# Kernel optimization log

Hardware: AMD Instinct MI355X
Metric: run time of the kernel (lower is better)

## Reference

```python
import jax, jax.numpy as jnp
import numpy as np

B, C, H, W = 16, 192, 48, 48
EPS = 1e-5  # torch LayerNorm default


def setup_inputs() -> dict:
    key = jax.random.key(0)
    ks = jax.random.split(key, 5)
    dim = C
    x = jax.random.normal(ks[0], (B, C, H, W), dtype=jnp.float32)
    ln_w = jnp.ones((dim,), dtype=jnp.float32)
    ln_b = jnp.zeros((dim,), dtype=jnp.float32)
    s = 1.0 / np.sqrt(dim)
    Wq = jax.random.uniform(ks[1], (dim, dim), jnp.float32, -s, s)
    Wk = jax.random.uniform(ks[2], (dim, dim), jnp.float32, -s, s)
    Wv = jax.random.uniform(ks[3], (dim, dim), jnp.float32, -s, s)
    w1 = jnp.ones((1,), dtype=jnp.float32)
    w2 = jnp.ones((1,), dtype=jnp.float32)
    return {"x": x, "ln_w": ln_w, "ln_b": ln_b, "Wq": Wq, "Wk": Wk, "Wv": Wv, "w1": w1, "w2": w2}


def reference(x, ln_w, ln_b, Wq, Wk, Wv, w1, w2):
    b, c, h, w = x.shape
    # [B, C, H, W] -> [B, N, C]
    xf = x.reshape(b, c, h * w).transpose(0, 2, 1)
    # LayerNorm over channel dim
    mu = jnp.mean(xf, axis=-1, keepdims=True)
    var = jnp.mean(jnp.square(xf - mu), axis=-1, keepdims=True)
    xn = (xf - mu) * jax.lax.rsqrt(var + EPS) * ln_w + ln_b
    # torch Linear: y = x @ W^T
    Q = jnp.einsum('bnc,dc->bnd', xn, Wq)
    K = jnp.einsum('bnc,dc->bnd', xn, Wk)
    V = jnp.einsum('bnc,dc->bnd', xn, Wv)
    S = jnp.einsum('bnd,bmd->bnm', Q, K)  # [B, N, N]
    attn1 = jax.nn.softmax(S, axis=-1)
    attn2 = jnp.square(jax.nn.relu(S))
    # learned blend weights (softmax over two scalars)
    e1, e2 = jnp.exp(w1), jnp.exp(w2)
    denom = e1 + e2
    attn = (e1 / denom) * attn1 + (e2 / denom) * attn2
    out = jnp.einsum('bnm,bmd->bnd', attn, V)  # [B, N, C]
    out = out.transpose(0, 2, 1).reshape(b, c, h, w)
    return out + x
```

## Files before the change

kernel.cpp:

```cpp
#include <hip/hip_runtime.h>

#define NN 2304
#define CC 192
#define NBATCH 16

typedef unsigned short u16;
typedef __bf16 bf16x8 __attribute__((ext_vector_type(8)));
typedef float f32x4 __attribute__((ext_vector_type(4)));
typedef float f32x16 __attribute__((ext_vector_type(16)));

__device__ __forceinline__ u16 bf16bits(float f) {
  union { float f; unsigned u; } v;
  v.f = f;
  unsigned r = v.u + 0x7FFFu + ((v.u >> 16) & 1u);
  return (u16)(r >> 16);
}

__device__ __forceinline__ int swzK(int row, int col) {
  int ch = col >> 3;
  int phys = (ch & ~7) | ((ch ^ row) & 7);
  return row * 192 + (phys << 3) + (col & 7);
}
__device__ __forceinline__ int swz64(int row, int col) {
  int ch = (col >> 3) ^ row;
  return (row << 6) | ((ch & 7) << 3) | (col & 7);
}

__device__ __forceinline__ void gll16(const u16* g, u16* l) {
  __builtin_amdgcn_global_load_lds(
      (const __attribute__((address_space(1))) u16*)g,
      (__attribute__((address_space(3))) u16*)l, 16, 0, 0);
}

__global__ __launch_bounds__(256) void ln_kernel(
    const float* __restrict__ x, const float* __restrict__ lnw,
    const float* __restrict__ lnb, u16* __restrict__ xn) {
  __shared__ float xt[192 * 65];
  __shared__ float psum[4][64], psq[4][64];
  __shared__ float mu_s[64], rs_s[64];
  __shared__ float lw_s[192], lb_s[192];
  int t = threadIdx.x;
  int b = blockIdx.y, n0 = blockIdx.x * 64;
  const float* xb = x + (size_t)b * CC * NN;
  if (t < 192) { lw_s[t] = lnw[t]; lb_s[t] = lnb[t]; }
#pragma unroll
  for (int i = 0; i < 48; ++i) {
    int idx = i * 256 + t;
    int c = idx >> 6, n = idx & 63;
    xt[c * 65 + n] = xb[(size_t)c * NN + n0 + n];
  }
  __syncthreads();
  {
    int n = t & 63, part = t >> 6;
    float s = 0.f, s2 = 0.f;
#pragma unroll
    for (int c = part * 48; c < part * 48 + 48; ++c) {
      float v = xt[c * 65 + n];
      s += v; s2 += v * v;
    }
    psum[part][n] = s; psq[part][n] = s2;
  }
  __syncthreads();
  if (t < 64) {
    float s = psum[0][t] + psum[1][t] + psum[2][t] + psum[3][t];
    float s2 = psq[0][t] + psq[1][t] + psq[2][t] + psq[3][t];
    float mu = s * (1.0f / 192.0f);
    float var = s2 * (1.0f / 192.0f) - mu * mu;
    mu_s[t] = mu;
    rs_s[t] = rsqrtf(var + 1e-5f);
  }
  __syncthreads();
#pragma unroll
  for (int i = 0; i < 12; ++i) {
    int u = i * 256 + t;
    int n = u / 48, cq = (u % 48) * 4;
    float mu = mu_s[n], rs = rs_s[n];
    alignas(8) u16 tmp[4];
#pragma unroll
    for (int k2 = 0; k2 < 4; ++k2) {
      float v = (xt[(cq + k2) * 65 + n] - mu) * rs * lw_s[cq + k2] + lb_s[cq + k2];
      tmp[k2] = bf16bits(v);
    }
    *(uint2*)&xn[((size_t)(b * NN + n0 + n)) * CC + cq] = *(uint2*)tmp;
  }
}

__global__ __launch_bounds__(256, 3) void qkv_gemm(
    const u16* __restrict__ xn, const float* __restrict__ Wq,
    const float* __restrict__ Wk, const float* __restrict__ Wv,
    u16* __restrict__ qb, u16* __restrict__ kb, u16* __restrict__ vtb) {
  __shared__ u16 xs[12288];
  __shared__ u16 wsm[12288];
  int t = threadIdx.x, w = t >> 6, lane = t & 63, l15 = lane & 15, qd = lane >> 4;
  int m0 = blockIdx.x * 64, n0 = blockIdx.y * 64, z = blockIdx.z;
  const float* W = (z == 0) ? Wq : (z == 1 ? Wk : Wv);
#pragma unroll
  for (int i = 0; i < 6; ++i) {
    int ch = i * 256 + t;
    int row = ch / 24, cin = (ch % 24) * 8;
    *(uint4*)&xs[swzK(row, cin)] = *(const uint4*)&xn[(size_t)(m0 + row) * 192 + cin];
  }
#pragma unroll
  for (int i = 0; i < 6; ++i) {
    int ch = i * 256 + t;
    int row = ch / 24, cin = (ch % 24) * 8;
    const float* src = &W[(size_t)(n0 + row) * 192 + cin];
    alignas(16) u16 tmp[8];
#pragma unroll
    for (int j = 0; j < 8; ++j) tmp[j] = bf16bits(src[j]);
    *(uint4*)&wsm[swzK(row, cin)] = *(uint4*)tmp;
  }
  __syncthreads();
  bf16x8 a[6];
#pragma unroll
  for (int kk = 0; kk < 6; ++kk)
    a[kk] = *(const bf16x8*)&xs[swzK(w * 16 + l15, kk * 32 + qd * 8)];
  const f32x4 fz = {0.f, 0.f, 0.f, 0.f};
  f32x4 acc[4];
#pragma unroll
  for (int ct = 0; ct < 4; ++ct) {
    acc[ct] = fz;
#pragma unroll
    for (int kk = 0; kk < 6; ++kk) {
      bf16x8 bfr = *(const bf16x8*)&wsm[swzK(ct * 16 + l15, kk * 32 + qd * 8)];
      acc[ct] = __builtin_amdgcn_mfma_f32_16x16x32_bf16(a[kk], bfr, acc[ct], 0, 0, 0);
    }
  }
  if (z < 2) {
    u16* outp = (z == 0) ? qb : kb;
#pragma unroll
    for (int ct = 0; ct < 4; ++ct)
#pragma unroll
      for (int r = 0; r < 4; ++r) {
        int m = m0 + w * 16 + qd * 4 + r;
        outp[(size_t)m * 192 + n0 + ct * 16 + l15] = bf16bits(acc[ct][r]);
      }
  } else {
    __syncthreads();
#pragma unroll
    for (int ct = 0; ct < 4; ++ct)
#pragma unroll
      for (int r = 0; r < 4; ++r)
        xs[swz64(ct * 16 + l15, w * 16 + qd * 4 + r)] = bf16bits(acc[ct][r]);
    __syncthreads();
    int b = blockIdx.x / 36, nb = (blockIdx.x % 36) * 64;
#pragma unroll
    for (int i = 0; i < 16; ++i) {
      int idx = i * 256 + t;
      int d = idx >> 6, nn = idx & 63;
      vtb[(size_t)b * 192 * NN + (size_t)(n0 + d) * NN + nb + nn] = xs[swz64(d, nn)];
    }
  }
}

__global__ __launch_bounds__(256, 3) void attn_lsum(
    const u16* __restrict__ qb, const u16* __restrict__ kb,
    float* __restrict__ lsum_g) {
  __shared__ u16 sm[24576];
  __shared__ float lp[2][2][32];
  int t = threadIdx.x, w = t >> 6, lane = t & 63;
  int l31 = lane & 31, hi = lane >> 5;
  int qh = w >> 1, ch = w & 1;
  int bid = blockIdx.x;
  int xcd = bid & 7, j = bid >> 3;
  int b = xcd * 2 + (j >= 36 ? 1 : 0);
  int qt = (j >= 36) ? j - 36 : j;

  const u16* Kg = kb + (size_t)b * NN * CC;
  const u16* Qr = qb + ((size_t)b * NN + qt * 64 + qh * 32 + l31) * CC + hi * 8;
  bf16x8 qf[12];
#pragma unroll
  for (int ks = 0; ks < 12; ++ks) qf[ks] = *(const bf16x8*)(Qr + ks * 16);

#pragma unroll
  for (int i = 0; i < 6; ++i) {
    int cid = i * 4 + w, sc = cid * 64 + lane;
    int row = sc / 24, pc = sc % 24;
    int gc = (pc & ~7) | ((pc ^ row) & 7);
    gll16(Kg + (size_t)row * CC + gc * 8, sm + cid * 512);
  }

  f32x16 z16;
#pragma unroll
  for (int i = 0; i < 16; ++i) z16[i] = 0.f;
  float lsum = 0.f;

  for (int kt = 0; kt < 36; ++kt) {
    asm volatile("s_waitcnt vmcnt(0) lgkmcnt(0)\ns_barrier" ::: "memory");
    if (kt + 1 < 36) {
      u16* dst = sm + ((kt + 1) & 1) * 12288;
#pragma unroll
      for (int i = 0; i < 6; ++i) {
        int cid = i * 4 + w, sc = cid * 64 + lane;
        int row = sc / 24, pc = sc % 24;
        int gc = (pc & ~7) | ((pc ^ row) & 7);
        gll16(Kg + ((size_t)(kt + 1) * 64 + row) * CC + gc * 8, dst + cid * 512);
      }
    }
    const u16* kl = sm + (kt & 1) * 12288;
    f32x16 s0 = z16, s1 = z16;
    __builtin_amdgcn_s_setprio(1);
#pragma unroll
    for (int ks = 0; ks < 6; ++ks) {
      bf16x8 k0 = *(const bf16x8*)&kl[swzK(ch * 32 + l31, (2 * ks) * 16 + hi * 8)];
      bf16x8 k1 = *(const bf16x8*)&kl[swzK(ch * 32 + l31, (2 * ks + 1) * 16 + hi * 8)];
      s0 = __builtin_amdgcn_mfma_f32_32x32x16_bf16(k0, qf[2 * ks], s0, 0, 0, 0);
      s1 = __builtin_amdgcn_mfma_f32_32x32x16_bf16(k1, qf[2 * ks + 1], s1, 0, 0, 0);
    }
    __builtin_amdgcn_s_setprio(0);
#pragma unroll
    for (int r = 0; r < 16; ++r) {
      float s = s0[r] + s1[r];
      lsum += __expf(fminf(s, 60.f));
    }
  }
  lsum += __shfl_xor(lsum, 32);
  if (lane < 32) lp[qh][ch][l31] = lsum;
  __syncthreads();
  if (w == 0) {
    lsum_g[(size_t)b * NN + qt * 64 + lane] =
        lp[lane >> 5][0][lane & 31] + lp[lane >> 5][1][lane & 31];
  }
}

__global__ __launch_bounds__(256, 2) void attn_pv(
    const u16* __restrict__ qb, const u16* __restrict__ kb,
    const u16* __restrict__ vtb, const float* __restrict__ lsum_g,
    const float* __restrict__ w1p, const float* __restrict__ w2p,
    const float* __restrict__ x, float* __restrict__ out) {
  __shared__ u16 sm[24576];
  float* olds = (float*)sm;

  int t = threadIdx.x, w = t >> 6, lane = t & 63;
  int l31 = lane & 31, hi = lane >> 5;
  int qh = w >> 1, ch = w & 1;
  int bid = blockIdx.x;
  int xcd = bid & 7, j = bid >> 3;
  int b = xcd * 2 + (j >= 36 ? 1 : 0);
  int qt = (j >= 36) ? j - 36 : j;

  const u16* Kg = kb + (size_t)b * NN * CC;
  const u16* Vg = vtb + (size_t)b * CC * NN;
  const u16* Qr = qb + ((size_t)b * NN + qt * 64 + qh * 32 + l31) * CC + hi * 8;
  bf16x8 qf[12];
#pragma unroll
  for (int ks = 0; ks < 12; ++ks) qf[ks] = *(const bf16x8*)(Qr + ks * 16);

  float e1 = __expf(w1p[0]), e2 = __expf(w2p[0]);
  float den = e1 + e2;
  float c2f = e2 / den;
  float cl1 = (e1 / den) / lsum_g[(size_t)b * NN + qt * 64 + qh * 32 + l31];

  f32x16 z16;
#pragma unroll
  for (int i = 0; i < 16; ++i) z16[i] = 0.f;
  f32x16 os[3];
#pragma unroll
  for (int i = 0; i < 3; ++i) os[i] = z16;

#define STAGE_K(KT)                                                        \
  {                                                                        \
    _Pragma("unroll") for (int i = 0; i < 6; ++i) {                        \
      int cid = i * 4 + w, sc = cid * 64 + lane;                           \
      int row = sc / 24, pc = sc % 24;                                     \
      int gc = (pc & ~7) | ((pc ^ row) & 7);                               \
      gll16(Kg + ((size_t)(KT) * 64 + row) * CC + gc * 8, sm + cid * 512); \
    }                                                                      \
  }
#define STAGE_V(KT)                                                        \
  {                                                                        \
    _Pragma("unroll") for (int i = 0; i < 6; ++i) {                        \
      int cid = i * 4 + w, sc = cid * 64 + lane;                           \
      int d = sc >> 3, pc = sc & 7, gc = (pc ^ d) & 7;                     \
      gll16(Vg + (size_t)d * NN + (KT) * 64 + gc * 8,                      \
            sm + 12288 + cid * 512);                                       \
    }                                                                      \
  }

  uint32_t pA[4][4];
#define S_BLEND()                                                           \
  {                                                                         \
    _Pragma("unroll") for (int kblk = 0; kblk < 2; ++kblk) {                \
      f32x16 sA = z16;                                                      \
      __builtin_amdgcn_s_setprio(1);                                        \
      _Pragma("unroll") for (int ks = 0; ks < 12; ++ks) {                   \
        bf16x8 kf =                                                         \
            *(const bf16x8*)&sm[swzK(kblk * 32 + l31, ks * 16 + hi * 8)];   \
        sA = __builtin_amdgcn_mfma_f32_32x32x16_bf16(kf, qf[ks], sA, 0, 0, 0); \
      }                                                                     \
      __builtin_amdgcn_s_setprio(0);                                        \
      uint32_t W[8];                                                        \
      _Pragma("unroll") for (int g = 0; g < 4; ++g) {                       \
        float sv0 = sA[4 * g + 0], sv1 = sA[4 * g + 1];                     \
        float sv2 = sA[4 * g + 2], sv3 = sA[4 * g + 3];                     \
        float p0 = cl1 * __expf(fminf(sv0, 60.f)) +                         \
                   c2f * ((sv0 > 0.f) ? sv0 * sv0 : 0.f);                   \
        float p1 = cl1 * __expf(fminf(sv1, 60.f)) +                         \
                   c2f * ((sv1 > 0.f) ? sv1 * sv1 : 0.f);                   \
        float p2 = cl1 * __expf(fminf(sv2, 60.f)) +                         \
                   c2f * ((sv2 > 0.f) ? sv2 * sv2 : 0.f);                   \
        float p3 = cl1 * __expf(fminf(sv3, 60.f)) +                         \
                   c2f * ((sv3 > 0.f) ? sv3 * sv3 : 0.f);                   \
        W[2 * g] = ((uint32_t)bf16bits(p1) << 16) | bf16bits(p0);           \
        W[2 * g + 1] = ((uint32_t)bf16bits(p3) << 16) | bf16bits(p2);       \
      }                                                                     \
      uint32_t X[8];                                                        \
      _Pragma("unroll") for (int jj = 0; jj < 8; ++jj)                      \
          X[jj] = __shfl_xor(W[jj], 32);                                    \
      pA[2 * kblk][0] = hi ? X[2] : W[0];                                   \
      pA[2 * kblk][1] = hi ? X[3] : W[1];                                   \
      pA[2 * kblk][2] = hi ? W[2] : X[0];                                   \
      pA[2 * kblk][3] = hi ? W[3] : X[1];                                   \
      pA[2 * kblk + 1][0] = hi ? X[6] : W[4];                               \
      pA[2 * kblk + 1][1] = hi ? X[7] : W[5];                               \
      pA[2 * kblk + 1][2] = hi ? W[6] : X[4];                               \
      pA[2 * kblk + 1][3] = hi ? W[7] : X[5];                               \
    }                                                                       \
  }

  STAGE_K(0);
  STAGE_V(0);
  asm volatile("s_waitcnt vmcnt(6)\ns_barrier" ::: "memory");
  S_BLEND();
  asm volatile("s_waitcnt lgkmcnt(0)\ns_barrier" ::: "memory");
  STAGE_K(1);

  for (int kt = 0; kt < 36; ++kt) {
    if (kt == 35)
      asm volatile("s_waitcnt vmcnt(0) lgkmcnt(0)\ns_barrier" ::: "memory");
    else
      asm volatile("s_waitcnt vmcnt(6) lgkmcnt(0)\ns_barrier" ::: "memory");

    const u16* vl = sm + 12288;
    __builtin_amdgcn_s_setprio(1);
#pragma unroll
    for (int dt = 0; dt < 3; ++dt) {
      int d = ch * 96 + dt * 32 + l31;
#pragma unroll
      for (int kk = 0; kk < 4; ++kk) {
        bf16x8 vf = *(const bf16x8*)&vl[swz64(d, kk * 16 + hi * 8)];
        os[dt] = __builtin_amdgcn_mfma_f32_32x32x16_bf16(
            *(const bf16x8*)pA[kk], vf, os[dt], 0, 0, 0);
      }
    }
    __builtin_amdgcn_s_setprio(0);

    if (kt < 35) {
      asm volatile("s_waitcnt vmcnt(0) lgkmcnt(0)\ns_barrier" ::: "memory");
      STAGE_V(kt + 1);
      S_BLEND();
      asm volatile("s_waitcnt lgkmcnt(0)\ns_barrier" ::: "memory");
      if (kt + 2 < 36) STAGE_K(kt + 2);
    }
  }

  __syncthreads();
#pragma unroll
  for (int dt = 0; dt < 3; ++dt) {
    int d = ch * 96 + dt * 32 + l31;
#pragma unroll
    for (int r = 0; r < 16; ++r) {
      int m = (r & 3) + 8 * (r >> 2) + 4 * hi;
      int q = qh * 32 + m;
      olds[d * 64 + ((q & ~31) | ((q ^ d) & 31))] = os[dt][r];
    }
  }
  __syncthreads();
  const float* xb = x + (size_t)b * CC * NN + qt * 64;
  float* ob = out + (size_t)b * CC * NN + qt * 64;
#pragma unroll
  for (int i = 0; i < 48; ++i) {
    int idx = i * 256 + t;
    int c = idx >> 6, nn = idx & 63;
    float v = olds[c * 64 + ((nn & ~31) | ((nn ^ c) & 31))];
    ob[(size_t)c * NN + nn] = v + xb[(size_t)c * NN + nn];
  }
#undef STAGE_K
#undef STAGE_V
#undef S_BLEND
}

extern "C" void kernel_launch(void* const* d_in, const int* in_sizes, int n_in,
                              void* d_out, int out_size, void* d_ws, size_t ws_size,
                              hipStream_t stream) {
  (void)in_sizes; (void)n_in; (void)out_size; (void)ws_size;
  const float* x   = (const float*)d_in[0];
  const float* lnw = (const float*)d_in[1];
  const float* lnb = (const float*)d_in[2];
  const float* Wq  = (const float*)d_in[3];
  const float* Wk  = (const float*)d_in[4];
  const float* Wv  = (const float*)d_in[5];
  const float* w1  = (const float*)d_in[6];
  const float* w2  = (const float*)d_in[7];
  float* out = (float*)d_out;

  u16* xn = (u16*)d_ws;
  size_t per = (size_t)NBATCH * NN * CC;
  u16* qb  = xn + per;
  u16* kb  = qb + per;
  u16* vtb = kb + per;
  float* lsum_g = (float*)d_ws;

  ln_kernel<<<dim3(36, 16), 256, 0, stream>>>(x, lnw, lnb, xn);
  qkv_gemm<<<dim3(576, 3, 3), 256, 0, stream>>>(xn, Wq, Wk, Wv, qb, kb, vtb);
  attn_lsum<<<dim3(576), 256, 0, stream>>>(qb, kb, lsum_g);
  attn_pv<<<dim3(576), 256, 0, stream>>>(qb, kb, vtb, lsum_g, w1, w2, x, out);
}
```

Before: 345.8 us.

## Split QK^T score tiles across wave pairs and exchange P via LDS

In the attention PV kernel, the two waves sharing a query half used to each compute the full 64-key score block, duplicating the QK^T MFMAs and the blend exp. Now each wave computes only its 32-key half, writes its packed bf16 probabilities to a new LDS exchange region, and reads the partner's half for the PV MFMAs. This halves the redundant score and softmax work at the cost of 8KB more LDS and extra LDS traffic. Bit-twiddled bf16 rounding is also replaced with the hardware v_cvt_pk_bf16_f32 instruction in the layernorm, weight-convert and blend paths.

```diff
diff --git a/kernel.cpp b/kernel.cpp
--- a/kernel.cpp
+++ b/kernel.cpp
@@ -14,6 +14,12 @@
   v.f = f;
   unsigned r = v.u + 0x7FFFu + ((v.u >> 16) & 1u);
   return (u16)(r >> 16);
+}
+
+__device__ __forceinline__ uint32_t cvtpk(float lo, float hi) {
+  uint32_t d;
+  asm("v_cvt_pk_bf16_f32 %0, %1, %2" : "=v"(d) : "v"(lo), "v"(hi));
+  return d;
 }
 
 __device__ __forceinline__ int swzK(int row, int col) {
@@ -75,13 +81,14 @@
     int u = i * 256 + t;
     int n = u / 48, cq = (u % 48) * 4;
     float mu = mu_s[n], rs = rs_s[n];
-    alignas(8) u16 tmp[4];
-#pragma unroll
-    for (int k2 = 0; k2 < 4; ++k2) {
-      float v = (xt[(cq + k2) * 65 + n] - mu) * rs * lw_s[cq + k2] + lb_s[cq + k2];
-      tmp[k2] = bf16bits(v);
-    }
-    *(uint2*)&xn[((size_t)(b * NN + n0 + n)) * CC + cq] = *(uint2*)tmp;
+    float v0 = (xt[(cq + 0) * 65 + n] - mu) * rs * lw_s[cq + 0] + lb_s[cq + 0];
+    float v1 = (xt[(cq + 1) * 65 + n] - mu) * rs * lw_s[cq + 1] + lb_s[cq + 1];
+    float v2 = (xt[(cq + 2) * 65 + n] - mu) * rs * lw_s[cq + 2] + lb_s[cq + 2];
+    float v3 = (xt[(cq + 3) * 65 + n] - mu) * rs * lw_s[cq + 3] + lb_s[cq + 3];
+    uint2 o;
+    o.x = cvtpk(v0, v1);
+    o.y = cvtpk(v2, v3);
+    *(uint2*)&xn[((size_t)(b * NN + n0 + n)) * CC + cq] = o;
   }
 }
 
@@ -105,10 +112,14 @@
     int ch = i * 256 + t;
     int row = ch / 24, cin = (ch % 24) * 8;
     const float* src = &W[(size_t)(n0 + row) * 192 + cin];
-    alignas(16) u16 tmp[8];
-#pragma unroll
-    for (int j = 0; j < 8; ++j) tmp[j] = bf16bits(src[j]);
-    *(uint4*)&wsm[swzK(row, cin)] = *(uint4*)tmp;
+    float4 f0 = *(const float4*)src;
+    float4 f1 = *(const float4*)(src + 4);
+    uint4 o;
+    o.x = cvtpk(f0.x, f0.y);
+    o.y = cvtpk(f0.z, f0.w);
+    o.z = cvtpk(f1.x, f1.y);
+    o.w = cvtpk(f1.z, f1.w);
+    *(uint4*)&wsm[swzK(row, cin)] = o;
   }
   __syncthreads();
   bf16x8 a[6];
@@ -228,7 +239,7 @@
     const u16* __restrict__ vtb, const float* __restrict__ lsum_g,
     const float* __restrict__ w1p, const float* __restrict__ w2p,
     const float* __restrict__ x, float* __restrict__ out) {
-  __shared__ u16 sm[24576];
+  __shared__ u16 sm[28672];
   float* olds = (float*)sm;
 
   int t = threadIdx.x, w = t >> 6, lane = t & 63;
@@ -250,6 +261,9 @@
   float den = e1 + e2;
   float c2f = e2 / den;
   float cl1 = (e1 / den) / lsum_g[(size_t)b * NN + qt * 64 + qh * 32 + l31];
+
+  u16* pexW = sm + 24576 + (qh * 2 + ch) * 1024 + lane * 8;
+  const u16* pexR = sm + 24576 + (qh * 2 + (1 - ch)) * 1024 + lane * 8;
 
   f32x16 z16;
 #pragma unroll
@@ -277,45 +291,44 @@
     }                                                                      \
   }
 
-  uint32_t pA[4][4];
+  alignas(16) uint32_t pOwn0[4], pOwn1[4];
 #define S_BLEND()                                                           \
   {                                                                         \
-    _Pragma("unroll") for (int kblk = 0; kblk < 2; ++kblk) {                \
-      f32x16 sA = z16;                                                      \
-      __builtin_amdgcn_s_setprio(1);                                        \
-      _Pragma("unroll") for (int ks = 0; ks < 12; ++ks) {                   \
-        bf16x8 kf =                                                         \
-            *(const bf16x8*)&sm[swzK(kblk * 32 + l31, ks * 16 + hi * 8)];   \
-        sA = __builtin_amdgcn_mfma_f32_32x32x16_bf16(kf, qf[ks], sA, 0, 0, 0); \
-      }                                                                     \
-      __builtin_amdgcn_s_setprio(0);                                        \
-      uint32_t W[8];                                                        \
-      _Pragma("unroll") for (int g = 0; g < 4; ++g) {                       \
-        float sv0 = sA[4 * g + 0], sv1 = sA[4 * g + 1];                     \
-        float sv2 = sA[4 * g + 2], sv3 = sA[4 * g + 3];                     \
-        float p0 = cl1 * __expf(fminf(sv0, 60.f)) +                         \
-                   c2f * ((sv0 > 0.f) ? sv0 * sv0 : 0.f);                   \
-        float p1 = cl1 * __expf(fminf(sv1, 60.f)) +                         \
-                   c2f * ((sv1 > 0.f) ? sv1 * sv1 : 0.f);                   \
-        float p2 = cl1 * __expf(fminf(sv2, 60.f)) +                         \
-                   c2f * ((sv2 > 0.f) ? sv2 * sv2 : 0.f);                   \
-        float p3 = cl1 * __expf(fminf(sv3, 60.f)) +                         \
-                   c2f * ((sv3 > 0.f) ? sv3 * sv3 : 0.f);                   \
-        W[2 * g] = ((uint32_t)bf16bits(p1) << 16) | bf16bits(p0);           \
-        W[2 * g + 1] = ((uint32_t)bf16bits(p3) << 16) | bf16bits(p2);       \
-      }                                                                     \
-      uint32_t X[8];                                                        \
-      _Pragma("unroll") for (int jj = 0; jj < 8; ++jj)                      \
-          X[jj] = __shfl_xor(W[jj], 32);                                    \
-      pA[2 * kblk][0] = hi ? X[2] : W[0];                                   \
-      pA[2 * kblk][1] = hi ? X[3] : W[1];                                   \
-      pA[2 * kblk][2] = hi ? W[2] : X[0];                                   \
-      pA[2 * kblk][3] = hi ? W[3] : X[1];                                   \
-      pA[2 * kblk + 1][0] = hi ? X[6] : W[4];                               \
-      pA[2 * kblk + 1][1] = hi ? X[7] : W[5];                               \
-      pA[2 * kblk + 1][2] = hi ? W[6] : X[4];                               \
-      pA[2 * kblk + 1][3] = hi ? W[7] : X[5];                               \
+    f32x16 sA0 = z16, sA1 = z16;                                            \
+    __builtin_amdgcn_s_setprio(1);                                          \
+    _Pragma("unroll") for (int ks = 0; ks < 6; ++ks) {                      \
+      bf16x8 k0 =                                                           \
+          *(const bf16x8*)&sm[swzK(ch * 32 + l31, (2 * ks) * 16 + hi * 8)]; \
+      bf16x8 k1 =                                                           \
+          *(const bf16x8*)&sm[swzK(ch * 32 + l31, (2 * ks + 1) * 16 + hi * 8)]; \
+      sA0 = __builtin_amdgcn_mfma_f32_32x32x16_bf16(k0, qf[2 * ks], sA0, 0, 0, 0); \
+      sA1 = __builtin_amdgcn_mfma_f32_32x32x16_bf16(k1, qf[2 * ks + 1], sA1, 0, 0, 0); \
     }                                                                       \
+    __builtin_amdgcn_s_setprio(0);                                          \
+    uint32_t W[8];                                                          \
+    _Pragma("unroll") for (int g = 0; g < 4; ++g) {                         \
+      float sv0 = sA0[4 * g + 0] + sA1[4 * g + 0];                          \
+      float sv1 = sA0[4 * g + 1] + sA1[4 * g + 1];                          \
+      float sv2 = sA0[4 * g + 2] + sA1[4 * g + 2];                          \
+      float sv3 = sA0[4 * g + 3] + sA1[4 * g + 3];                          \
+      float r0 = fmaxf(sv0, 0.f), r1 = fmaxf(sv1, 0.f);                     \
+      float r2 = fmaxf(sv2, 0.f), r3 = fmaxf(sv3, 0.f);                     \
+      float p0 = cl1 * __expf(fminf(sv0, 60.f)) + c2f * r0 * r0;            \
+      float p1 = cl1 * __expf(fminf(sv1, 60.f)) + c2f * r1 * r1;            \
+      float p2 = cl1 * __expf(fminf(sv2, 60.f)) + c2f * r2 * r2;            \
+      float p3 = cl1 * __expf(fminf(sv3, 60.f)) + c2f * r3 * r3;            \
+      W[2 * g] = cvtpk(p0, p1);                                             \
+      W[2 * g + 1] = cvtpk(p2, p3);                                         \
+    }                                                                       \
+    uint32_t X[8];                                                          \
+    _Pragma("unroll") for (int jj = 0; jj < 8; ++jj)                        \
+        X[jj] = __shfl_xor(W[jj], 32);                                      \
+    pOwn0[0] = hi ? X[2] : W[0]; pOwn0[1] = hi ? X[3] : W[1];               \
+    pOwn0[2] = hi ? W[2] : X[0]; pOwn0[3] = hi ? W[3] : X[1];               \
+    pOwn1[0] = hi ? X[6] : W[4]; pOwn1[1] = hi ? X[7] : W[5];               \
+    pOwn1[2] = hi ? W[6] : X[4]; pOwn1[3] = hi ? W[7] : X[5];               \
+    *(uint4*)pexW = *(uint4*)pOwn0;                                         \
+    *(uint4*)(pexW + 512) = *(uint4*)pOwn1;                                 \
   }
 
   STAGE_K(0);
@@ -332,16 +345,24 @@
       asm volatile("s_waitcnt vmcnt(6) lgkmcnt(0)\ns_barrier" ::: "memory");
 
     const u16* vl = sm + 12288;
+    uint4 pb0 = *(const uint4*)pexR;
+    uint4 pb1 = *(const uint4*)(pexR + 512);
     __builtin_amdgcn_s_setprio(1);
 #pragma unroll
     for (int dt = 0; dt < 3; ++dt) {
       int d = ch * 96 + dt * 32 + l31;
-#pragma unroll
-      for (int kk = 0; kk < 4; ++kk) {
-        bf16x8 vf = *(const bf16x8*)&vl[swz64(d, kk * 16 + hi * 8)];
-        os[dt] = __builtin_amdgcn_mfma_f32_32x32x16_bf16(
-            *(const bf16x8*)pA[kk], vf, os[dt], 0, 0, 0);
-      }
+      bf16x8 vo0 = *(const bf16x8*)&vl[swz64(d, (ch * 2 + 0) * 16 + hi * 8)];
+      bf16x8 vo1 = *(const bf16x8*)&vl[swz64(d, (ch * 2 + 1) * 16 + hi * 8)];
+      bf16x8 vs0 = *(const bf16x8*)&vl[swz64(d, ((1 - ch) * 2 + 0) * 16 + hi * 8)];
+      bf16x8 vs1 = *(const bf16x8*)&vl[swz64(d, ((1 - ch) * 2 + 1) * 16 + hi * 8)];
+      os[dt] = __builtin_amdgcn_mfma_f32_32x32x16_bf16(
+          *(const bf16x8*)pOwn0, vo0, os[dt], 0, 0, 0);
+      os[dt] = __builtin_amdgcn_mfma_f32_32x32x16_bf16(
+          *(const bf16x8*)pOwn1, vo1, os[dt], 0, 0, 0);
+      os[dt] = __builtin_amdgcn_mfma_f32_32x32x16_bf16(
+          *(const bf16x8*)&pb0, vs0, os[dt], 0, 0, 0);
+      os[dt] = __builtin_amdgcn_mfma_f32_32x32x16_bf16(
+          *(const bf16x8*)&pb1, vs1, os[dt], 0, 0, 0);
     }
     __builtin_amdgcn_s_setprio(0);
 
```

Measured after the change: 295.3 us. -14.6%, faster.
